# Optimization experiments

Hardware: AMD Instinct MI355X
Metric: run time of the kernel (lower is better)

The kernel has to match this reference:

```python
import jax, jax.numpy as jnp
import numpy as np

D = 256; DFF = 1024; H = 8; L = 4; P = 4; NK = 18; NQ = 100; BS = 8; DH = D // H
SHAPES = ((100, 100), (50, 50), (25, 25), (13, 13))   # (H_l, W_l) per level
START = (0, 10000, 12500, 13125); LIN = 13294
PARAM_SHAPES = [
    ("across_in_w", (3 * D, D)), ("across_in_b", (3 * D,)), ("across_out_w", (D, D)), ("across_out_b", (D,)),
    ("within_in_w", (3 * D, D)), ("within_in_b", (3 * D,)), ("within_out_w", (D, D)), ("within_out_b", (D,)),
    ("off_w", (H * L * P * 2, D)), ("off_b", (H * L * P * 2,)), ("aw_w", (H * L * P, D)), ("aw_b", (H * L * P,)),
    ("val_w", (D, D)), ("val_b", (D,)), ("msout_w", (D, D)), ("msout_b", (D,)),
    ("lin1_w", (DFF, D)), ("lin1_b", (DFF,)), ("lin2_w", (D, DFF)), ("lin2_b", (D,)),
    ("lin1p_w", (DFF, D)), ("lin1p_b", (DFF,)), ("lin2p_w", (D, DFF)), ("lin2p_b", (D,)),
]
NORMS = ["across_norm", "within_norm", "norm1", "norm2", "norm2p"]
PNAMES = [n for n, _ in PARAM_SHAPES] + [n + s for n in NORMS for s in ("_g", "_b")]


def setup_inputs():
    ks = iter(jax.random.split(jax.random.key(0), 80))
    rn = lambda s, sc=1.0: jax.random.normal(next(ks), s, jnp.float32) * sc
    inp = {}
    inp["tgt_pose"] = rn((NQ, BS, NK, D))
    inp["tgt_pose_query_pos"] = rn((NQ, BS, NK, D))
    inp["tgt_pose_reference_points"] = jax.random.uniform(next(ks), (NQ * NK, BS, L, 2), jnp.float32)
    inp["memory"] = rn((LIN, BS, D))
    for n, s in PARAM_SHAPES:
        inp[n] = rn(s, 0.02)
    for n in NORMS:
        inp[n + "_g"] = 1.0 + rn((D,), 0.02)
        inp[n + "_b"] = rn((D,), 0.02)
    return inp


def _ln(x, g, b):
    mu = x.mean(-1, keepdims=True)
    xc = x - mu
    return xc * jax.lax.rsqrt((xc * xc).mean(-1, keepdims=True) + 1e-5) * g + b


def _mha(q, k, v, in_w, in_b, out_w, out_b, mask=None):
    # q,k,v: [S,B,D] (torch nn.MultiheadAttention layout)
    S, B, _ = q.shape
    def proj(x, i):
        return (x @ in_w[i * D:(i + 1) * D].T + in_b[i * D:(i + 1) * D]).reshape(-1, B, H, DH).transpose(1, 2, 0, 3)
    qh = proj(q, 0) * (DH ** -0.5); kh = proj(k, 1); vh = proj(v, 2)   # [B,H,S,DH]
    sc = jnp.einsum('bhqd,bhkd->bhqk', qh, kh)
    if mask is not None:
        sc = sc + mask
    o = jnp.einsum('bhqk,bhkd->bhqd', jax.nn.softmax(sc, -1), vh)
    return o.transpose(2, 0, 1, 3).reshape(S, B, D) @ out_w.T + out_b


def _msdeform(query, ref, mem, off_w, off_b, aw_w, aw_b, val_w, val_b, out_w, out_b):
    # query [N,Lq,D], ref [N,Lq,L,2] in [0,1] (x,y), mem [N,LIN,D]
    N, Lq, _ = query.shape
    value = (mem @ val_w.T + val_b).reshape(N, LIN, H, DH).transpose(0, 2, 1, 3)   # [N,H,LIN,DH]
    off = (query @ off_w.T + off_b).reshape(N, Lq, H, L, P, 2)
    aw = jax.nn.softmax((query @ aw_w.T + aw_b).reshape(N, Lq, H, L * P), -1).reshape(N, Lq, H, L, P)
    normalizer = jnp.array([[w, h] for (h, w) in SHAPES], jnp.float32)   # (W_l, H_l)
    loc = ref[:, :, None, :, None, :] + off / normalizer[None, None, None, :, None, :]   # [N,Lq,H,L,P,2]
    lvl_outs = []
    for li, (Hl, Wl) in enumerate(SHAPES):
        v_l = value[:, :, START[li]:START[li] + Hl * Wl]   # [N,H,Hl*Wl,DH]
        g = loc[:, :, :, li]                               # [N,Lq,H,P,2]
        # grid_sample(align_corners=False, padding_mode='zeros') on sampling grid 2*loc-1
        x = g[..., 0] * Wl - 0.5; y = g[..., 1] * Hl - 0.5
        x0 = jnp.floor(x); y0 = jnp.floor(y)
        lx = x - x0; ly = y - y0
        x0i = x0.astype(jnp.int32); y0i = y0.astype(jnp.int32)
        def gather(xi, yi):
            valid = ((xi >= 0) & (xi < Wl) & (yi >= 0) & (yi < Hl)).astype(v_l.dtype)
            idx = jnp.clip(yi, 0, Hl - 1) * Wl + jnp.clip(xi, 0, Wl - 1)   # [N,Lq,H,P]
            it = idx.transpose(0, 2, 1, 3).reshape(N, H, Lq * P)
            vt = jnp.take_along_axis(v_l, it[..., None], axis=2).reshape(N, H, Lq, P, DH)
            return vt * valid.transpose(0, 2, 1, 3)[..., None]
        wx = lx.transpose(0, 2, 1, 3)[..., None]; wy = ly.transpose(0, 2, 1, 3)[..., None]
        samp = (gather(x0i, y0i) * (1 - wx) * (1 - wy) + gather(x0i + 1, y0i) * wx * (1 - wy)
                + gather(x0i, y0i + 1) * (1 - wx) * wy + gather(x0i + 1, y0i + 1) * wx * wy)
        lvl_outs.append(samp)   # [N,H,Lq,P,DH]
    samp = jnp.stack(lvl_outs, 0)   # [L,N,H,Lq,P,DH]
    out = jnp.einsum('lnhqpd,nqhlp->nqhd', samp, aw).reshape(N, Lq, D)
    return out @ out_w.T + out_b


def _forward(tgt, pos, ref, mem, p):
    # 1) across-person self-attention along nq
    qf = tgt.reshape(NQ, BS * NK, D)
    t2 = _mha(qf, qf, qf, p['across_in_w'], p['across_in_b'], p['across_out_w'], p['across_out_b']).reshape(NQ, BS, NK, D)
    tgt = _ln(tgt + t2, p['across_norm_g'], p['across_norm_b'])
    # 2) deformable cross-attention; with_pos_embed mutates tgt in place in the original
    tgt = tgt + pos
    q = tgt.transpose(1, 0, 2, 3).reshape(BS, NQ * NK, D)
    t2 = _msdeform(q, ref.transpose(1, 0, 2, 3), mem.transpose(1, 0, 2),
                   p['off_w'], p['off_b'], p['aw_w'], p['aw_b'], p['val_w'], p['val_b'], p['msout_w'], p['msout_b'])
    t2 = t2.reshape(BS, NQ, NK, D).transpose(1, 0, 2, 3)
    tgt = _ln(tgt + t2, p['norm1_g'], p['norm1_b'])
    # 3) FFN
    t2 = jax.nn.relu(tgt @ p['lin1_w'].T + p['lin1_b']) @ p['lin2_w'].T + p['lin2_b']
    tgt = _ln(tgt + t2, p['norm2_g'], p['norm2_b'])
    # 4) within-pose self-attention (second in-place with_pos_embed)
    tgt = tgt + pos
    qw = tgt.reshape(NQ * BS, NK, D).transpose(1, 0, 2)
    mask = jnp.full((NK, NK), 1e-8, tgt.dtype)   # zero adjacency matrix additive mask
    t2 = _mha(qw, qw, qw, p['within_in_w'], p['within_in_b'], p['within_out_w'], p['within_out_b'], mask)
    t2 = t2.transpose(1, 0, 2).reshape(NQ, BS, NK, D)
    tgt = _ln(tgt + t2, p['within_norm_g'], p['within_norm_b'])
    # 5) late FFN
    t2 = jax.nn.relu(tgt @ p['lin1p_w'].T + p['lin1p_b']) @ p['lin2p_w'].T + p['lin2p_b']
    return _ln(tgt + t2, p['norm2p_g'], p['norm2p_b'])


def reference(tgt_pose, tgt_pose_query_pos, tgt_pose_reference_points, memory, across_in_w, across_in_b, across_out_w, across_out_b, within_in_w, within_in_b, within_out_w, within_out_b, off_w, off_b, aw_w, aw_b, val_w, val_b, msout_w, msout_b, lin1_w, lin1_b, lin2_w, lin2_b, lin1p_w, lin1p_b, lin2p_w, lin2p_b, across_norm_g, across_norm_b, within_norm_g, within_norm_b, norm1_g, norm1_b, norm2_g, norm2_b, norm2p_g, norm2p_b):
    _l = dict(locals())
    p = {n: _l[n] for n in PNAMES}
    return _forward(tgt_pose, tgt_pose_query_pos, tgt_pose_reference_points, memory, p)
```

## Files before the change

kernel.cpp:

```cpp
#include <hip/hip_runtime.h>
#include <cstdint>
#include <cstddef>

constexpr int D_   = 256;
constexpr int NK_  = 18;
constexpr int NQ_  = 100;
constexpr int BS_  = 8;
constexpr int T_   = NQ_ * BS_ * NK_;
constexpr int LIN_ = 13294;
constexpr int LQ_  = NQ_ * NK_;

typedef __attribute__((ext_vector_type(8))) short bfv8;
typedef __attribute__((ext_vector_type(4))) float f32x4;

__device__ __forceinline__ ushort f2b(float f) {
  uint32_t u = __builtin_bit_cast(uint32_t, f);
  u += 0x7fffu + ((u >> 16) & 1u);
  return (ushort)(u >> 16);
}
__device__ __forceinline__ float b2f(ushort h) {
  uint32_t u = ((uint32_t)h) << 16;
  return __builtin_bit_cast(float, u);
}
__device__ __forceinline__ uint pk2(float lo, float hi) {
  return (uint)f2b(lo) | ((uint)f2b(hi) << 16);
}
__device__ __forceinline__ void gload16(const ushort* g, ushort* l) {
  __builtin_amdgcn_global_load_lds(
      (const __attribute__((address_space(1))) void*)g,
      (__attribute__((address_space(3))) void*)l, 16, 0, 0);
}

constexpr int WOF0  = 0;
constexpr int WOF1  = 196608;
constexpr int WOF2  = 393216;
constexpr int WOF3  = 458752;
constexpr int WOF4  = 524288;
constexpr int WOF5  = 589824;
constexpr int WOF6  = 622592;
constexpr int WOF7  = 688128;
constexpr int WOF8  = 753664;
constexpr int WOF9  = 1015808;
constexpr int WOF10 = 1277952;
constexpr int WOF11 = 1540096;
constexpr int WTOT  = 1802240;

__global__ __launch_bounds__(256) void conv_weights(
    const float* __restrict__ w0, const float* __restrict__ w1,
    const float* __restrict__ w2, const float* __restrict__ w3,
    const float* __restrict__ w4, const float* __restrict__ w5,
    const float* __restrict__ w6, const float* __restrict__ w7,
    const float* __restrict__ w8, const float* __restrict__ w9,
    const float* __restrict__ w10, const float* __restrict__ w11,
    ushort* __restrict__ out,
    const float* __restrict__ off_b, const float* __restrict__ aw_b,
    float* __restrict__ oab) {
  if (blockIdx.x == 0) {
    int t = threadIdx.x;
    oab[t] = (t < 256) ? off_b[t] : aw_b[t - 256];
    oab[t + 128] = (t + 128 < 256) ? off_b[t + 128] : aw_b[t - 128];
  }
  int i8 = (blockIdx.x * 256 + threadIdx.x) * 8;
  if (i8 >= WTOT) return;
  const float* src; int off;
  if      (i8 < WOF1)  { src = w0;  off = WOF0; }
  else if (i8 < WOF2)  { src = w1;  off = WOF1; }
  else if (i8 < WOF3)  { src = w2;  off = WOF2; }
  else if (i8 < WOF4)  { src = w3;  off = WOF3; }
  else if (i8 < WOF5)  { src = w4;  off = WOF4; }
  else if (i8 < WOF6)  { src = w5;  off = WOF5; }
  else if (i8 < WOF7)  { src = w6;  off = WOF6; }
  else if (i8 < WOF8)  { src = w7;  off = WOF7; }
  else if (i8 < WOF9)  { src = w8;  off = WOF8; }
  else if (i8 < WOF10) { src = w9;  off = WOF9; }
  else if (i8 < WOF11) { src = w10; off = WOF10; }
  else                 { src = w11; off = WOF11; }
  const float4 v0 = *(const float4*)(src + (i8 - off));
  const float4 v1 = *(const float4*)(src + (i8 - off) + 4);
  uint4 o;
  o.x = pk2(v0.x, v0.y); o.y = pk2(v0.z, v0.w);
  o.z = pk2(v1.x, v1.y); o.w = pk2(v1.z, v1.w);
  *(uint4*)(out + i8) = o;
}

__global__ __launch_bounds__(256) void conv_acts(
    const float* __restrict__ mem, ushort* __restrict__ memb,
    const float* __restrict__ tgt, ushort* __restrict__ tgtb) {
  int idx = blockIdx.x * 256 + threadIdx.x;
  int r = idx >> 5, c = (idx & 31) * 8;
  const int MV = BS_ * LIN_;
  const float* p;
  ushort* q;
  if (r < MV) {
    int i = r >> 3, b = r & 7;
    p = mem + (size_t)r * 256 + c;
    q = memb + ((size_t)b * LIN_ + i) * 256 + c;
  } else {
    int rr = r - MV;
    if (rr >= T_) return;
    p = tgt + (size_t)rr * 256 + c;
    q = tgtb + (size_t)rr * 256 + c;
  }
  float4 v0 = *(const float4*)p, v1 = *(const float4*)(p + 4);
  uint4 o;
  o.x = pk2(v0.x, v0.y); o.y = pk2(v0.z, v0.w);
  o.z = pk2(v1.x, v1.y); o.w = pk2(v1.z, v1.w);
  *(uint4*)q = o;
}

template<int AMODE, int OUTMODE, int BM>
__global__ __launch_bounds__(256) void gemm_mfma(
    const ushort* __restrict__ A, const ushort* __restrict__ W,
    const float* __restrict__ bias, void* __restrict__ Cv,
    int M, int N, int K) {
  constexpr int AJ = BM / 64;
  constexpr int MR = BM / 32;
  __shared__ ushort As[BM * 32];
  __shared__ ushort Bs[128 * 32];
  const int tid = threadIdx.x;
  const int bm = blockIdx.y * BM, bn = blockIdx.x * 128;
  const int wave = tid >> 6, lane = tid & 63;

  const int srow = wave * 16 + (lane >> 2);
  const ushort* gA[AJ]; ushort* lA[AJ];
  const ushort* gB[2];  ushort* lB[2];
#pragma unroll
  for (int j = 0; j < AJ; ++j) {
    int row = j * 64 + srow;
    int gch = (lane & 3) ^ (row & 3);
    int gm = bm + row; if (gm >= M) gm = M - 1;
    int asrc;
    if (AMODE == 0) {
      asrc = gm;
    } else {
      int b = gm / LQ_, lq = gm - b * LQ_;
      int qq = lq / NK_, kk = lq - qq * NK_;
      asrc = qq * (BS_ * NK_) + b * NK_ + kk;
    }
    gA[j] = A + (size_t)asrc * K + gch * 8;
    lA[j] = As + (j * 4 + wave) * 512;
  }
#pragma unroll
  for (int j = 0; j < 2; ++j) {
    int row = j * 64 + srow;
    int gch = (lane & 3) ^ (row & 3);
    gB[j] = W + (size_t)(bn + row) * K + gch * 8;
    lB[j] = Bs + (j * 4 + wave) * 512;
  }

  const int wm = (wave >> 1) * (BM / 2), wn = (wave & 1) * 64;
  const int fr = lane & 15, fk = lane >> 4;
  const int sw = (fk ^ (fr & 3)) << 3;

  f32x4 acc[MR][4] = {};
  for (int k0 = 0; k0 < K; k0 += 32) {
#pragma unroll
    for (int j = 0; j < AJ; ++j) gload16(gA[j] + k0, lA[j]);
#pragma unroll
    for (int j = 0; j < 2; ++j) gload16(gB[j] + k0, lB[j]);
    __syncthreads();
    bfv8 a[MR], b[4];
#pragma unroll
    for (int m = 0; m < MR; ++m)
      a[m] = *(const bfv8*)&As[(wm + m * 16 + fr) * 32 + sw];
#pragma unroll
    for (int n = 0; n < 4; ++n)
      b[n] = *(const bfv8*)&Bs[(wn + n * 16 + fr) * 32 + sw];
#pragma unroll
    for (int m = 0; m < MR; ++m)
#pragma unroll
      for (int n = 0; n < 4; ++n)
        acc[m][n] = __builtin_amdgcn_mfma_f32_16x16x32_bf16(a[m], b[n], acc[m][n], 0, 0, 0);
    __syncthreads();
  }

  const int row0 = (lane >> 4) * 4;
  const int col = lane & 15;
#pragma unroll
  for (int m = 0; m < MR; ++m) {
#pragma unroll
    for (int n = 0; n < 4; ++n) {
      int cn = bn + wn + n * 16 + col;
      float bv = bias[cn];
#pragma unroll
      for (int j = 0; j < 4; ++j) {
        int mg = bm + wm + m * 16 + row0 + j;
        if (mg < M) {
          float o = acc[m][n][j] + bv;
          if (OUTMODE == 2) o = fmaxf(o, 0.f);
          if (OUTMODE == 0) ((float*)Cv)[(size_t)mg * N + cn] = o;
          else ((ushort*)Cv)[(size_t)mg * N + cn] = f2b(o);
        }
      }
    }
  }
}

template<int LNMODE>
__global__ __launch_bounds__(256) void gemm_ln(
    const ushort* __restrict__ A, const ushort* __restrict__ W,
    const float* __restrict__ bias, const ushort* __restrict__ Xb,
    const float* __restrict__ POS, const float* __restrict__ G,
    const float* __restrict__ Bb, void* __restrict__ Out, int K) {
  __shared__ float Ep[32][264];
  ushort* As = (ushort*)&Ep[0][0];
  ushort* Bs = As + 32 * 32;

  const int tid = threadIdx.x;
  const int wave = tid >> 6, lane = tid & 63;
  const int bm = blockIdx.x * 32;

  const int arow = wave * 8 + (lane >> 2);
  const int agch = (lane & 3) ^ (arow & 3);
  const ushort* gA = A + (size_t)(bm + arow) * K + agch * 8;
  ushort* lA = As + wave * 256;
  const int srow = wave * 16 + (lane >> 2);
  const ushort* gB[4]; ushort* lB[4];
#pragma unroll
  for (int j = 0; j < 4; ++j) {
    int row = j * 64 + srow;
    int gch = (lane & 3) ^ (row & 3);
    gB[j] = W + (size_t)row * K + gch * 8;
    lB[j] = Bs + (j * 4 + wave) * 512;
  }

  const int wn = wave * 64;
  const int fr = lane & 15, fk = lane >> 4;
  const int sw = (fk ^ (fr & 3)) << 3;

  f32x4 acc[2][4] = {};
  for (int k0 = 0; k0 < K; k0 += 32) {
    if (lane < 32) gload16(gA + k0, lA);
#pragma unroll
    for (int j = 0; j < 4; ++j) gload16(gB[j] + k0, lB[j]);
    __syncthreads();
    bfv8 a[2], b[4];
#pragma unroll
    for (int m = 0; m < 2; ++m)
      a[m] = *(const bfv8*)&As[(m * 16 + fr) * 32 + sw];
#pragma unroll
    for (int n = 0; n < 4; ++n)
      b[n] = *(const bfv8*)&Bs[(wn + n * 16 + fr) * 32 + sw];
#pragma unroll
    for (int m = 0; m < 2; ++m)
#pragma unroll
      for (int n = 0; n < 4; ++n)
        acc[m][n] = __builtin_amdgcn_mfma_f32_16x16x32_bf16(a[m], b[n], acc[m][n], 0, 0, 0);
    __syncthreads();
  }

  const int row0 = (lane >> 4) * 4;
  const int col = lane & 15;
  float bv[4];
#pragma unroll
  for (int n = 0; n < 4; ++n) bv[n] = bias[wn + n * 16 + col];

  const float4 g4 = *(const float4*)(G + lane * 4);
  const float4 bb4 = *(const float4*)(Bb + lane * 4);

#pragma unroll
  for (int m = 0; m < 2; ++m)
#pragma unroll
    for (int n = 0; n < 4; ++n)
#pragma unroll
      for (int j = 0; j < 4; ++j)
        Ep[m * 16 + row0 + j][wn + n * 16 + col] = acc[m][n][j] + bv[n];
  __syncthreads();

  for (int rr = 0; rr < 8; ++rr) {
    int lrow = wave * 8 + rr;
    size_t off = (size_t)(bm + lrow) * 256 + lane * 4;
    float4 ev = *(const float4*)&Ep[lrow][lane * 4];
    ushort4 x4 = *(const ushort4*)(Xb + off);
    float4 v = make_float4(b2f(x4.x) + ev.x, b2f(x4.y) + ev.y,
                           b2f(x4.z) + ev.z, b2f(x4.w) + ev.w);
    float s = v.x + v.y + v.z + v.w;
#pragma unroll
    for (int o = 32; o; o >>= 1) s += __shfl_xor(s, o);
    float mu = s * (1.0f / 256.0f);
    float4 c = make_float4(v.x - mu, v.y - mu, v.z - mu, v.w - mu);
    float q = c.x * c.x + c.y * c.y + c.z * c.z + c.w * c.w;
#pragma unroll
    for (int o = 32; o; o >>= 1) q += __shfl_xor(q, o);
    float rs = rsqrtf(q * (1.0f / 256.0f) + 1e-5f);
    float4 o4;
    o4.x = c.x * rs * g4.x + bb4.x;
    o4.y = c.y * rs * g4.y + bb4.y;
    o4.z = c.z * rs * g4.z + bb4.z;
    o4.w = c.w * rs * g4.w + bb4.w;
    if (LNMODE == 0) {
      float4 pv = *(const float4*)(POS + off);
      o4.x += pv.x; o4.y += pv.y; o4.z += pv.z; o4.w += pv.w;
    }
    if (LNMODE == 2) {
      *(float4*)((float*)Out + off) = o4;
    } else {
      ushort4 ob;
      ob.x = f2b(o4.x); ob.y = f2b(o4.y); ob.z = f2b(o4.z); ob.w = f2b(o4.w);
      *(ushort4*)((ushort*)Out + off) = ob;
    }
  }
}

__global__ __launch_bounds__(256) void attn_across_mfma(
    const ushort* __restrict__ QKV, ushort* __restrict__ O) {
  __shared__ ushort Qs[112][40];
  __shared__ ushort Ks[112][40];
  __shared__ ushort Vt[32][136];
  __shared__ ushort Ps[112][136];
  const int b = blockIdx.x >> 3, h = blockIdx.x & 7;
  const int tid = threadIdx.x;

  for (int idx = tid; idx < 112 * 16; idx += 256) {
    int r = idx >> 4, du = (idx & 15) * 2;
    uint q = 0, k = 0;
    if (r < 100) {
      size_t base = ((size_t)r * 144 + b) * 768 + h * 32 + du;
      q = *(const uint*)(QKV + base);
      k = *(const uint*)(QKV + base + 256);
    }
    *(uint*)&Qs[r][du] = q;
    *(uint*)&Ks[r][du] = k;
  }
  for (int idx = tid; idx < 128 * 32; idx += 256) {
    int s = idx >> 5, d = idx & 31;
    ushort v = 0;
    if (s < 100) v = QKV[((size_t)s * 144 + b) * 768 + 512 + h * 32 + d];
    Vt[d][s] = v;
  }
  for (int idx = tid; idx < 112 * 8; idx += 256) {
    int r = idx >> 3, c = 112 + (idx & 7) * 2;
    *(uint*)&Ps[r][c] = 0;
  }
  __syncthreads();

  const int wave = tid >> 6, lane = tid & 63;
  const int fr = lane & 15, fk = lane >> 4;
  const float scale = 0.17677669529663687f;

#pragma unroll
  for (int mi = 0; mi < 2; ++mi) {
    const int mt = wave + mi * 4;
    if (mt < 7) {
      bfv8 aq = *(const bfv8*)&Qs[mt * 16 + fr][fk * 8];
      f32x4 sacc[7];
#pragma unroll
      for (int nt = 0; nt < 7; ++nt) {
        bfv8 bk = *(const bfv8*)&Ks[nt * 16 + fr][fk * 8];
        f32x4 z = {0.f, 0.f, 0.f, 0.f};
        sacc[nt] = __builtin_amdgcn_mfma_f32_16x16x32_bf16(aq, bk, z, 0, 0, 0);
      }
      const bool maskc = (lane & 15) >= 4;
#pragma unroll
      for (int j = 0; j < 4; ++j) {
        float v[7];
        float mx = -1e30f;
#pragma unroll
        for (int nt = 0; nt < 7; ++nt) {
          float s = sacc[nt][j] * scale;
          if (nt == 6 && maskc) s = -1e30f;
          v[nt] = s;
          mx = fmaxf(mx, s);
        }
        mx = fmaxf(mx, __shfl_xor(mx, 1));
        mx = fmaxf(mx, __shfl_xor(mx, 2));
        mx = fmaxf(mx, __shfl_xor(mx, 4));
        mx = fmaxf(mx, __shfl_xor(mx, 8));
        float sum = 0.f;
#pragma unroll
        for (int nt = 0; nt < 7; ++nt) {
          v[nt] = __expf(v[nt] - mx);
          sum += v[nt];
        }
        sum += __shfl_xor(sum, 1);
        sum += __shfl_xor(sum, 2);
        sum += __shfl_xor(sum, 4);
        sum += __shfl_xor(sum, 8);
        float inv = 1.f / sum;
        int row = mt * 16 + (lane >> 4) * 4 + j;
#pragma unroll
        for (int nt = 0; nt < 7; ++nt)
          Ps[row][nt * 16 + (lane & 15)] = f2b(v[nt] * inv);
      }
    }
  }
  __syncthreads();

  f32x4 oacc[2][2] = {};
#pragma unroll
  for (int mi = 0; mi < 2; ++mi) {
    const int mt = wave + mi * 4;
    if (mt < 7) {
#pragma unroll
      for (int ks = 0; ks < 4; ++ks) {
        bfv8 ap = *(const bfv8*)&Ps[mt * 16 + fr][ks * 32 + fk * 8];
#pragma unroll
        for (int n = 0; n < 2; ++n) {
          bfv8 bv = *(const bfv8*)&Vt[n * 16 + fr][ks * 32 + fk * 8];
          oacc[mi][n] = __builtin_amdgcn_mfma_f32_16x16x32_bf16(ap, bv, oacc[mi][n], 0, 0, 0);
        }
      }
#pragma unroll
      for (int n = 0; n < 2; ++n) {
#pragma unroll
        for (int j = 0; j < 4; ++j) {
          int q = mt * 16 + (lane >> 4) * 4 + j;
          if (q < 100) {
            O[((size_t)q * 144 + b) * 256 + h * 32 + n * 16 + (lane & 15)] =
                f2b(oacc[mi][n][j]);
          }
        }
      }
    }
  }
}

__global__ __launch_bounds__(256) void attn_within(
    const ushort* __restrict__ QKV, ushort* __restrict__ O) {
  constexpr int ST = 258;
  __shared__ ushort Qs[18 * ST];
  __shared__ ushort Ks[18 * ST];
  __shared__ ushort Vs[18 * ST];
  const int bidx = blockIdx.x;
  const int qq = bidx >> 3, bb = bidx & 7;
  const int tid = threadIdx.x;
  for (int idx = tid; idx < 18 * 128; idx += 256) {
    int r = idx >> 7, j2 = (idx & 127) * 2;
    size_t base = ((size_t)qq * 144 + bb * 18 + r) * 768 + j2;
    *(uint*)&Qs[r * ST + j2] = *(const uint*)(QKV + base);
    *(uint*)&Ks[r * ST + j2] = *(const uint*)(QKV + base + 256);
    *(uint*)&Vs[r * ST + j2] = *(const uint*)(QKV + base + 512);
  }
  __syncthreads();
  const int wave = tid >> 6, lane = tid & 63;
  const int h = wave * 2 + (lane >> 5);
  const int li = lane & 31;
  const int hd = h * 32;
  const float scale = 0.17677669529663687f;
  const bool kv = li < 18;
  for (int s = 0; s < 18; ++s) {
    float sc = 0.f;
    if (kv) {
      const ushort* qrow = &Qs[s * ST + hd];
      const ushort* krow = &Ks[li * ST + hd];
#pragma unroll 8
      for (int d = 0; d < 32; ++d) sc += b2f(qrow[d]) * b2f(krow[d]);
    }
    sc = kv ? sc * scale : -1e30f;
    float mx = sc;
    mx = fmaxf(mx, __shfl_xor(mx, 16));
    mx = fmaxf(mx, __shfl_xor(mx, 8));
    mx = fmaxf(mx, __shfl_xor(mx, 4));
    mx = fmaxf(mx, __shfl_xor(mx, 2));
    mx = fmaxf(mx, __shfl_xor(mx, 1));
    float e = kv ? __expf(sc - mx) : 0.f;
    float sum = e;
    sum += __shfl_xor(sum, 16);
    sum += __shfl_xor(sum, 8);
    sum += __shfl_xor(sum, 4);
    sum += __shfl_xor(sum, 2);
    sum += __shfl_xor(sum, 1);
    float p = e / sum;
    float o = 0.f;
    const int half = lane & 32;
#pragma unroll
    for (int k = 0; k < 18; ++k) {
      float pk = __shfl(p, half + k);
      o += pk * b2f(Vs[k * ST + hd + li]);
    }
    O[((size_t)qq * 144 + bb * 18 + s) * 256 + hd + li] = f2b(o);
  }
}

__global__ __launch_bounds__(256) void deform_sample(
    const float* __restrict__ OFFAW, const ushort* __restrict__ V,
    const float* __restrict__ REF, ushort* __restrict__ OUT) {
  __shared__ uint2 sDesc[32 * 65];
  const int tid = threadIdx.x;
  const int m0 = blockIdx.x * 4;

  const int WH[4] = {100, 50, 25, 13};
  const int STl[4] = {0, 10000, 12500, 13125};

#pragma unroll
  for (int dd = 0; dd < 2; ++dd) {
    const int desc = tid + dd * 256;
    const int g = desc >> 7, rem = desc & 127;
    const int h = rem >> 4, lp = rem & 15, li = lp >> 2, p = lp & 3;
    const int m = m0 + g;
    const int b = m / LQ_, lq = m - b * LQ_;

    float awv = OFFAW[(size_t)m * 384 + 256 + h * 16 + lp];
    float mx = awv;
    mx = fmaxf(mx, __shfl_xor(mx, 8, 16));
    mx = fmaxf(mx, __shfl_xor(mx, 4, 16));
    mx = fmaxf(mx, __shfl_xor(mx, 2, 16));
    mx = fmaxf(mx, __shfl_xor(mx, 1, 16));
    float e = __expf(awv - mx);
    float sm = e;
    sm += __shfl_xor(sm, 8, 16);
    sm += __shfl_xor(sm, 4, 16);
    sm += __shfl_xor(sm, 2, 16);
    sm += __shfl_xor(sm, 1, 16);
    const float aw = e / sm;

    const float* offp = OFFAW + (size_t)m * 384 + h * 32 + li * 8 + p * 2;
    const float ox = offp[0], oy = offp[1];
    const float rx = REF[(((size_t)lq * 8 + b) * 4 + li) * 2 + 0];
    const float ry = REF[(((size_t)lq * 8 + b) * 4 + li) * 2 + 1];
    const int Wl = WH[li], st = STl[li];
    const float fW = (float)Wl;
    const float x = fmaf(rx, fW, ox) - 0.5f;
    const float y = fmaf(ry, fW, oy) - 0.5f;
    const float x0f = floorf(x), y0f = floorf(y);
    const float lx = x - x0f, ly = y - y0f;
    const int x0 = (int)x0f, y0 = (int)y0f;
    const int base = (g * 8 + h) * 65 + lp * 4;
#pragma unroll
    for (int c = 0; c < 4; ++c) {
      const int cx = c & 1, cy = c >> 1;
      const int xi = x0 + cx, yi = y0 + cy;
      const bool va = (xi >= 0) && (xi < Wl) && (yi >= 0) && (yi < Wl);
      const int xc = min(max(xi, 0), Wl - 1);
      const int yc = min(max(yi, 0), Wl - 1);
      const float wx = cx ? lx : (1.f - lx);
      const float wy = cy ? ly : (1.f - ly);
      const float wgt = va ? aw * wx * wy : 0.f;
      uint2 dv;
      dv.x = (uint)(st + yc * Wl + xc);
      dv.y = __builtin_bit_cast(uint, wgt);
      sDesc[base + c] = dv;
    }
  }
  __syncthreads();

  const int g = tid >> 6;
  const int h = (tid >> 3) & 7;
  const int d4 = (tid & 7) * 4;
  const int m = m0 + g;
  const int b = m / LQ_, lq = m - b * LQ_;
  const int qq = lq / NK_, kk = lq - qq * NK_;
  const ushort* Vg = V + ((size_t)b * LIN_) * 256 + h * 32 + d4;
  const int dbase = (g * 8 + h) * 65;
  float a0 = 0.f, a1 = 0.f, a2 = 0.f, a3 = 0.f;
#pragma unroll
  for (int lp = 0; lp < 16; ++lp) {
#pragma unroll
    for (int c = 0; c < 4; ++c) {
      const uint2 dv = sDesc[dbase + lp * 4 + c];
      const float w = __builtin_bit_cast(float, dv.y);
      const ushort4 v = *(const ushort4*)(Vg + (size_t)dv.x * 256);
      a0 = fmaf(w, b2f(v.x), a0);
      a1 = fmaf(w, b2f(v.y), a1);
      a2 = fmaf(w, b2f(v.z), a2);
      a3 = fmaf(w, b2f(v.w), a3);
    }
  }
  const size_t tok = (size_t)qq * 144 + b * 18 + kk;
  ushort4 o;
  o.x = f2b(a0); o.y = f2b(a1); o.z = f2b(a2); o.w = f2b(a3);
  *(ushort4*)(OUT + tok * 256 + h * 32 + d4) = o;
}

extern "C" void kernel_launch(void* const* d_in, const int* in_sizes, int n_in,
                              void* d_out, int out_size, void* d_ws, size_t ws_size,
                              hipStream_t stream) {
  const float* tgt  = (const float*)d_in[0];
  const float* pos  = (const float*)d_in[1];
  const float* ref  = (const float*)d_in[2];
  const float* mem  = (const float*)d_in[3];
  const float* across_in_w  = (const float*)d_in[4];
  const float* across_in_b  = (const float*)d_in[5];
  const float* across_out_w = (const float*)d_in[6];
  const float* across_out_b = (const float*)d_in[7];
  const float* within_in_w  = (const float*)d_in[8];
  const float* within_in_b  = (const float*)d_in[9];
  const float* within_out_w = (const float*)d_in[10];
  const float* within_out_b = (const float*)d_in[11];
  const float* off_w  = (const float*)d_in[12];
  const float* off_b  = (const float*)d_in[13];
  const float* aw_w   = (const float*)d_in[14];
  const float* aw_b   = (const float*)d_in[15];
  const float* val_w  = (const float*)d_in[16];
  const float* val_b  = (const float*)d_in[17];
  const float* msout_w = (const float*)d_in[18];
  const float* msout_b = (const float*)d_in[19];
  const float* lin1_w  = (const float*)d_in[20];
  const float* lin1_b  = (const float*)d_in[21];
  const float* lin2_w  = (const float*)d_in[22];
  const float* lin2_b  = (const float*)d_in[23];
  const float* lin1p_w = (const float*)d_in[24];
  const float* lin1p_b = (const float*)d_in[25];
  const float* lin2p_w = (const float*)d_in[26];
  const float* lin2p_b = (const float*)d_in[27];
  const float* across_norm_g = (const float*)d_in[28];
  const float* across_norm_b = (const float*)d_in[29];
  const float* within_norm_g = (const float*)d_in[30];
  const float* within_norm_b = (const float*)d_in[31];
  const float* norm1_g = (const float*)d_in[32];
  const float* norm1_b = (const float*)d_in[33];
  const float* norm2_g = (const float*)d_in[34];
  const float* norm2_b = (const float*)d_in[35];
  const float* norm2p_g = (const float*)d_in[36];
  const float* norm2p_b = (const float*)d_in[37];

  char* w = (char*)d_ws;
  ushort* Wb    = (ushort*)w;  w += 3604480;
  ushort* R1    = (ushort*)w;  w += (size_t)(BS_ * LIN_) * 256 * 2;
  ushort* AOb   = (ushort*)w;  w += (size_t)T_ * 256 * 2;
  ushort* CTb   = (ushort*)w;  w += (size_t)T_ * 256 * 2;
  ushort* Vb    = (ushort*)w;  w += (size_t)(BS_ * LIN_) * 256 * 2;
  float*  R2    = (float*)w;   w += (size_t)T_ * 384 * 4;
  float*  OAB   = (float*)w;   w += 384 * 4;
  ushort* memb  = R1;
  ushort* QKVb  = R1;
  ushort* tgtb  = (ushort*)R2;
  float*  OFFAW = R2;
  ushort* Uff   = Vb;
  ushort* SMPb  = AOb;

  ushort* W_across_in  = Wb + WOF0;
  ushort* W_within_in  = Wb + WOF1;
  ushort* W_across_out = Wb + WOF2;
  ushort* W_within_out = Wb + WOF3;
  ushort* W_offaw      = Wb + WOF4;
  ushort* W_val        = Wb + WOF6;
  ushort* W_msout      = Wb + WOF7;
  ushort* W_lin1       = Wb + WOF8;
  ushort* W_lin2       = Wb + WOF9;
  ushort* W_lin1p      = Wb + WOF10;
  ushort* W_lin2p      = Wb + WOF11;

  dim3 blk(256);
  const int MT = T_;
  const int MV = BS_ * LIN_;
  const int MVt = (MV + 127) / 128;
  const int MT64 = MT / 64;
  const int MT32 = MT / 32;

  conv_weights<<<dim3((WTOT / 8 + 255) / 256), blk, 0, stream>>>(
      across_in_w, within_in_w, across_out_w, within_out_w, off_w, aw_w,
      val_w, msout_w, lin1_w, lin2_w, lin1p_w, lin2p_w, Wb, off_b, aw_b, OAB);
  conv_acts<<<dim3(((MV + MT) * 32 + 255) / 256), blk, 0, stream>>>(
      mem, memb, tgt, tgtb);
  gemm_mfma<0, 1, 128><<<dim3(2, MVt), blk, 0, stream>>>(
      memb, W_val, val_b, Vb, MV, 256, 256);
  gemm_mfma<0, 1, 64><<<dim3(6, MT64), blk, 0, stream>>>(
      tgtb, W_across_in, across_in_b, QKVb, MT, 768, 256);
  attn_across_mfma<<<dim3(144 * 8), blk, 0, stream>>>(QKVb, AOb);
  gemm_ln<0><<<dim3(MT32), blk, 0, stream>>>(
      AOb, W_across_out, across_out_b, tgtb, pos,
      across_norm_g, across_norm_b, CTb, 256);
  gemm_mfma<2, 0, 64><<<dim3(3, MT64), blk, 0, stream>>>(
      CTb, W_offaw, OAB, OFFAW, MT, 384, 256);
  deform_sample<<<dim3(T_ / 4), blk, 0, stream>>>(OFFAW, Vb, ref, SMPb);
  gemm_ln<1><<<dim3(MT32), blk, 0, stream>>>(
      SMPb, W_msout, msout_b, CTb, nullptr,
      norm1_g, norm1_b, CTb, 256);
  gemm_mfma<0, 2, 64><<<dim3(8, MT64), blk, 0, stream>>>(
      CTb, W_lin1, lin1_b, Uff, MT, 1024, 256);
  gemm_ln<0><<<dim3(MT32), blk, 0, stream>>>(
      Uff, W_lin2, lin2_b, CTb, pos,
      norm2_g, norm2_b, CTb, 1024);
  gemm_mfma<0, 1, 64><<<dim3(6, MT64), blk, 0, stream>>>(
      CTb, W_within_in, within_in_b, QKVb, MT, 768, 256);
  attn_within<<<dim3(NQ_ * BS_), blk, 0, stream>>>(QKVb, AOb);
  gemm_ln<1><<<dim3(MT32), blk, 0, stream>>>(
      AOb, W_within_out, within_out_b, CTb, nullptr,
      within_norm_g, within_norm_b, CTb, 256);
  gemm_mfma<0, 2, 64><<<dim3(8, MT64), blk, 0, stream>>>(
      CTb, W_lin1p, lin1p_b, Uff, MT, 1024, 256);
  gemm_ln<2><<<dim3(MT32), blk, 0, stream>>>(
      Uff, W_lin2p, lin2p_b, CTb, nullptr,
      norm2p_g, norm2p_b, (float*)d_out, 1024);
}
```

Before: 379.8 us.

## Fuse FFN lin1+ReLU+lin2+LayerNorm into one kernel keeping hidden in LDS

Adds an ffn_ln kernel in which each 16-row block computes the 1024-wide ReLU hidden activation into shared memory and then runs the second GEMM, bias, residual and LayerNorm without leaving the kernel. Both FFN pairs now use it, so the bf16 hidden tensor is never written to or read back from global memory and one launch per FFN is dropped. In exchange, the 16-row tile means every block streams the full W1 and W2 through L2. The single-buffered loads with two barriers per k-step also give little overlap and poor weight reuse.

```diff
diff --git a/kernel.cpp b/kernel.cpp
--- a/kernel.cpp
+++ b/kernel.cpp
@@ -271,6 +271,141 @@
     int lrow = wave * 8 + rr;
     size_t off = (size_t)(bm + lrow) * 256 + lane * 4;
     float4 ev = *(const float4*)&Ep[lrow][lane * 4];
+    ushort4 x4 = *(const ushort4*)(Xb + off);
+    float4 v = make_float4(b2f(x4.x) + ev.x, b2f(x4.y) + ev.y,
+                           b2f(x4.z) + ev.z, b2f(x4.w) + ev.w);
+    float s = v.x + v.y + v.z + v.w;
+#pragma unroll
+    for (int o = 32; o; o >>= 1) s += __shfl_xor(s, o);
+    float mu = s * (1.0f / 256.0f);
+    float4 c = make_float4(v.x - mu, v.y - mu, v.z - mu, v.w - mu);
+    float q = c.x * c.x + c.y * c.y + c.z * c.z + c.w * c.w;
+#pragma unroll
+    for (int o = 32; o; o >>= 1) q += __shfl_xor(q, o);
+    float rs = rsqrtf(q * (1.0f / 256.0f) + 1e-5f);
+    float4 o4;
+    o4.x = c.x * rs * g4.x + bb4.x;
+    o4.y = c.y * rs * g4.y + bb4.y;
+    o4.z = c.z * rs * g4.z + bb4.z;
+    o4.w = c.w * rs * g4.w + bb4.w;
+    if (LNMODE == 0) {
+      float4 pv = *(const float4*)(POS + off);
+      o4.x += pv.x; o4.y += pv.y; o4.z += pv.z; o4.w += pv.w;
+    }
+    if (LNMODE == 2) {
+      *(float4*)((float*)Out + off) = o4;
+    } else {
+      ushort4 ob;
+      ob.x = f2b(o4.x); ob.y = f2b(o4.y); ob.z = f2b(o4.z); ob.w = f2b(o4.w);
+      *(ushort4*)((ushort*)Out + off) = ob;
+    }
+  }
+}
+
+template<int LNMODE>
+__global__ __launch_bounds__(256) void ffn_ln(
+    const ushort* __restrict__ A, const ushort* __restrict__ W1,
+    const float* __restrict__ b1, const ushort* __restrict__ W2,
+    const float* __restrict__ b2, const ushort* __restrict__ Xb,
+    const float* __restrict__ POS, const float* __restrict__ G,
+    const float* __restrict__ Bb, void* __restrict__ Out) {
+  __shared__ ushort As[16 * 256];
+  __shared__ ushort Hs[16 * 1024];
+  __shared__ ushort Bs[256 * 32];
+  float* Ep = (float*)Hs;
+
+  const int tid = threadIdx.x;
+  const int wave = tid >> 6, lane = tid & 63;
+  const int bm = blockIdx.x * 16;
+
+  {
+    int row = lane >> 2;
+    int gch = (lane & 3) ^ (row & 3);
+    const ushort* ga = A + (size_t)(bm + row) * 256 + gch * 8;
+#pragma unroll
+    for (int ti = 0; ti < 2; ++ti) {
+      int t = wave * 2 + ti;
+      gload16(ga + t * 32, As + t * 512);
+    }
+  }
+  const int srow = wave * 16 + (lane >> 2);
+  const int bgch = (lane & 3) ^ (srow & 3);
+  ushort* lB[4];
+#pragma unroll
+  for (int j = 0; j < 4; ++j) lB[j] = Bs + (j * 4 + wave) * 512;
+
+  const int wn = wave * 64;
+  const int fr = lane & 15, fk = lane >> 4;
+  const int sw = (fk ^ (fr & 3)) << 3;
+  const int row0 = (lane >> 4) * 4;
+  const int col = lane & 15;
+
+  for (int nc = 0; nc < 4; ++nc) {
+    f32x4 acc[4] = {};
+    for (int k0 = 0; k0 < 256; k0 += 32) {
+#pragma unroll
+      for (int j = 0; j < 4; ++j) {
+        int row = nc * 256 + j * 64 + srow;
+        gload16(W1 + (size_t)row * 256 + bgch * 8 + k0, lB[j]);
+      }
+      __syncthreads();
+      bfv8 a = *(const bfv8*)&As[(k0 >> 5) * 512 + fr * 32 + sw];
+      bfv8 b[4];
+#pragma unroll
+      for (int n = 0; n < 4; ++n)
+        b[n] = *(const bfv8*)&Bs[(wn + n * 16 + fr) * 32 + sw];
+#pragma unroll
+      for (int n = 0; n < 4; ++n)
+        acc[n] = __builtin_amdgcn_mfma_f32_16x16x32_bf16(a, b[n], acc[n], 0, 0, 0);
+      __syncthreads();
+    }
+#pragma unroll
+    for (int n = 0; n < 4; ++n) {
+      int cc = nc * 256 + wn + n * 16 + col;
+      float bv = b1[cc];
+#pragma unroll
+      for (int j = 0; j < 4; ++j) {
+        int hr = row0 + j;
+        float v = fmaxf(acc[n][j] + bv, 0.f);
+        Hs[hr * 1024 + (((cc >> 3) ^ (hr & 7)) << 3) + (cc & 7)] = f2b(v);
+      }
+    }
+  }
+
+  f32x4 acc2[4] = {};
+  for (int k0 = 0; k0 < 1024; k0 += 32) {
+#pragma unroll
+    for (int j = 0; j < 4; ++j) {
+      int row = j * 64 + srow;
+      gload16(W2 + (size_t)row * 1024 + bgch * 8 + k0, lB[j]);
+    }
+    __syncthreads();
+    bfv8 a = *(const bfv8*)&Hs[fr * 1024 + ((((k0 >> 3) + fk) ^ (fr & 7)) << 3)];
+    bfv8 b[4];
+#pragma unroll
+    for (int n = 0; n < 4; ++n)
+      b[n] = *(const bfv8*)&Bs[(wn + n * 16 + fr) * 32 + sw];
+#pragma unroll
+    for (int n = 0; n < 4; ++n)
+      acc2[n] = __builtin_amdgcn_mfma_f32_16x16x32_bf16(a, b[n], acc2[n], 0, 0, 0);
+    __syncthreads();
+  }
+
+  const float4 g4 = *(const float4*)(G + lane * 4);
+  const float4 bb4 = *(const float4*)(Bb + lane * 4);
+#pragma unroll
+  for (int n = 0; n < 4; ++n) {
+    float bv = b2[wn + n * 16 + col];
+#pragma unroll
+    for (int j = 0; j < 4; ++j)
+      Ep[(row0 + j) * 264 + wn + n * 16 + col] = acc2[n][j] + bv;
+  }
+  __syncthreads();
+
+  for (int rr = 0; rr < 4; ++rr) {
+    int lrow = wave * 4 + rr;
+    size_t off = (size_t)(bm + lrow) * 256 + lane * 4;
+    float4 ev = *(const float4*)&Ep[lrow * 264 + lane * 4];
     ushort4 x4 = *(const ushort4*)(Xb + off);
     float4 v = make_float4(b2f(x4.x) + ev.x, b2f(x4.y) + ev.y,
                            b2f(x4.z) + ev.z, b2f(x4.w) + ev.w);
@@ -616,7 +751,6 @@
   ushort* QKVb  = R1;
   ushort* tgtb  = (ushort*)R2;
   float*  OFFAW = R2;
-  ushort* Uff   = Vb;
   ushort* SMPb  = AOb;
 
   ushort* W_across_in  = Wb + WOF0;
@@ -637,6 +771,7 @@
   const int MVt = (MV + 127) / 128;
   const int MT64 = MT / 64;
   const int MT32 = MT / 32;
+  const int MT16 = MT / 16;
 
   conv_weights<<<dim3((WTOT / 8 + 255) / 256), blk, 0, stream>>>(
       across_in_w, within_in_w, across_out_w, within_out_w, off_w, aw_w,
@@ -657,20 +792,16 @@
   gemm_ln<1><<<dim3(MT32), blk, 0, stream>>>(
       SMPb, W_msout, msout_b, CTb, nullptr,
       norm1_g, norm1_b, CTb, 256);
-  gemm_mfma<0, 2, 64><<<dim3(8, MT64), blk, 0, stream>>>(
-      CTb, W_lin1, lin1_b, Uff, MT, 1024, 256);
-  gemm_ln<0><<<dim3(MT32), blk, 0, stream>>>(
-      Uff, W_lin2, lin2_b, CTb, pos,
-      norm2_g, norm2_b, CTb, 1024);
+  ffn_ln<0><<<dim3(MT16), blk, 0, stream>>>(
+      CTb, W_lin1, lin1_b, W_lin2, lin2_b, CTb, pos,
+      norm2_g, norm2_b, CTb);
   gemm_mfma<0, 1, 64><<<dim3(6, MT64), blk, 0, stream>>>(
       CTb, W_within_in, within_in_b, QKVb, MT, 768, 256);
   attn_within<<<dim3(NQ_ * BS_), blk, 0, stream>>>(QKVb, AOb);
   gemm_ln<1><<<dim3(MT32), blk, 0, stream>>>(
       AOb, W_within_out, within_out_b, CTb, nullptr,
       within_norm_g, within_norm_b, CTb, 256);
-  gemm_mfma<0, 2, 64><<<dim3(8, MT64), blk, 0, stream>>>(
-      CTb, W_lin1p, lin1p_b, Uff, MT, 1024, 256);
-  gemm_ln<2><<<dim3(MT32), blk, 0, stream>>>(
-      Uff, W_lin2p, lin2p_b, CTb, nullptr,
-      norm2p_g, norm2p_b, (float*)d_out, 1024);
-}
+  ffn_ln<2><<<dim3(MT16), blk, 0, stream>>>(
+      CTb, W_lin1p, lin1p_b, W_lin2p, lin2p_b, CTb, nullptr,
+      norm2p_g, norm2p_b, (float*)d_out);
+}
```

Result: slower. 410.9 us (+8.2%).
